# Kernel tuning notes

Hardware: AMD Instinct MI355X
Metric: run time of the kernel (lower is better)

The kernel has to match this reference:

```python
import jax, jax.numpy as jnp
import numpy as np

I_DIM = 50000
D_DIM = 128
N_EDGES = 800000
N_NODES = I_DIM + 1


def setup_inputs() -> dict:
    key = jax.random.key(0)
    k1, k2, k3, k4 = jax.random.split(key, 4)
    # edge[:,0] must be sorted for the original bincount+repeat normalization to be valid
    src = jnp.sort(jax.random.randint(k1, (N_EDGES,), 0, N_NODES))
    dst = jax.random.randint(k2, (N_EDGES,), 0, N_NODES)
    edge = jnp.stack([src, dst], axis=1).astype(jnp.int64)
    # GlorotNormal-style init for the embedding table and dense layers
    emb_mat = jax.random.normal(k3, (N_NODES, D_DIM), dtype=jnp.float32) * np.sqrt(2.0 / (N_NODES + D_DIM))
    kA, kB = jax.random.split(k4)
    W_scale = jax.random.normal(kA, (D_DIM, D_DIM), dtype=jnp.float32) * np.sqrt(2.0 / (2 * D_DIM))
    b_scale = jnp.zeros((D_DIM,), dtype=jnp.float32)
    W_att = jax.random.normal(kB, (2 * D_DIM, 1), dtype=jnp.float32) * np.sqrt(2.0 / (2 * D_DIM + 1))
    b_att = jnp.zeros((1,), dtype=jnp.float32)
    return {"edge": edge, "emb_mat": emb_mat, "W_scale": W_scale,
            "b_scale": b_scale, "W_att": W_att, "b_att": b_att}


def reference(edge, emb_mat, W_scale, b_scale, W_att, b_att):
    E = edge.shape[0]
    src = edge[:, 0]
    dst = edge[:, 1]
    # gather both endpoints, project: [E, 2, d]
    edge_emb = jnp.einsum('epd,df->epf', emb_mat[edge], W_scale) + b_scale
    edge_emb = edge_emb.reshape(E, -1)                       # [E, 2d]
    att = edge_emb @ W_att + b_att                           # [E, 1]
    att = jnp.where(att >= 0, att, 0.2 * att)                # LeakyReLU(0.2)
    att = jnp.squeeze(att, axis=-1)                          # [E]
    scores = jnp.exp(att - 1.0)
    score_sum = jax.ops.segment_sum(scores, src, num_segments=N_NODES)
    score_norm = scores / score_sum[src]                     # segment softmax
    item_scaled = emb_mat @ W_scale + b_scale                # [N, d]
    msgs = score_norm[:, None] * item_scaled[dst]            # [E, d]
    agg = jax.ops.segment_sum(msgs, src, num_segments=N_NODES)
    return jax.nn.sigmoid(agg)                               # [N, d]
```

## Files before the change

### kernel.cpp

```cpp
#include <hip/hip_runtime.h>
#include <math.h>

#define NN 50001
#define DD 128
#define NE 800000

typedef __attribute__((ext_vector_type(8))) short short8;
typedef __attribute__((ext_vector_type(4))) float floatx4;

__device__ __forceinline__ unsigned short f2bf(float f) {
    unsigned u = __builtin_bit_cast(unsigned, f);
    u += 0x7fffu + ((u >> 16) & 1u);
    return (unsigned short)(u >> 16);
}
__device__ __forceinline__ float bflo(unsigned u) {
    return __builtin_bit_cast(float, u << 16);
}
__device__ __forceinline__ float bfhi(unsigned u) {
    return __builtin_bit_cast(float, u & 0xffff0000u);
}

__global__ void k_prep(const float* __restrict__ W, unsigned short* __restrict__ WT,
                       const int* __restrict__ edge, int* __restrict__ row_ptr) {
    int b = blockIdx.x;
    if (b < 64) {
        int idx = b * 256 + threadIdx.x;
        int k = idx >> 7, j = idx & 127;
        WT[j * DD + k] = f2bf(W[idx]);
    } else {
        int e = (b - 64) * 256 + threadIdx.x;
        if (e >= NE) return;
        int s = edge[2 * e];
        if (e == 0) {
            for (int n = 0; n <= s; n++) row_ptr[n] = 0;
        } else {
            int p = edge[2 * (e - 1)];
            for (int n = p + 1; n <= s; n++) row_ptr[n] = e;
        }
        if (e == NE - 1) {
            for (int n = s + 1; n <= NN; n++) row_ptr[n] = NE;
        }
    }
}

__global__ void __launch_bounds__(256) k_gemm(const float* __restrict__ emb,
        const unsigned short* __restrict__ WT, const float* __restrict__ b_scale,
        const float* __restrict__ W_att, unsigned short* __restrict__ item,
        float* __restrict__ a_src, float* __restrict__ a_dst) {
    int wave = blockIdx.x * 4 + (threadIdx.x >> 6);
    int lane = threadIdx.x & 63;
    int base = wave * 16;
    if (base >= NN) return;
    int m = lane & 15, q = lane >> 4;

    int row = base + m; if (row >= NN) row = NN - 1;
    const float* ap = emb + (long)row * DD + q * 8;
    short8 a[4];
    #pragma unroll
    for (int ks = 0; ks < 4; ks++) {
        float4 f0 = *(const float4*)(ap + ks * 32);
        float4 f1 = *(const float4*)(ap + ks * 32 + 4);
        a[ks][0] = (short)f2bf(f0.x); a[ks][1] = (short)f2bf(f0.y);
        a[ks][2] = (short)f2bf(f0.z); a[ks][3] = (short)f2bf(f0.w);
        a[ks][4] = (short)f2bf(f1.x); a[ks][5] = (short)f2bf(f1.y);
        a[ks][6] = (short)f2bf(f1.z); a[ks][7] = (short)f2bf(f1.w);
    }

    float p_src[4] = {0.f, 0.f, 0.f, 0.f};
    float p_dst[4] = {0.f, 0.f, 0.f, 0.f};

    #pragma unroll
    for (int ft = 0; ft < 8; ft++) {
        int col = ft * 16 + m;
        floatx4 acc = {0.f, 0.f, 0.f, 0.f};
        #pragma unroll
        for (int ks = 0; ks < 4; ks++) {
            short8 b = *(const short8*)(WT + col * DD + ks * 32 + q * 8);
            acc = __builtin_amdgcn_mfma_f32_16x16x32_bf16(a[ks], b, acc, 0, 0, 0);
        }
        float bs = b_scale[col];
        float wsrc = W_att[col], wdst = W_att[DD + col];
        #pragma unroll
        for (int r = 0; r < 4; r++) {
            float v = acc[r] + bs;
            int gr = base + q * 4 + r;
            if (gr < NN) item[(long)gr * DD + col] = f2bf(v);
            p_src[r] += v * wsrc;
            p_dst[r] += v * wdst;
        }
    }
    #pragma unroll
    for (int off = 1; off <= 8; off <<= 1) {
        #pragma unroll
        for (int r = 0; r < 4; r++) {
            p_src[r] += __shfl_xor(p_src[r], off, 64);
            p_dst[r] += __shfl_xor(p_dst[r], off, 64);
        }
    }
    if (m == 0) {
        #pragma unroll
        for (int r = 0; r < 4; r++) {
            int gr = base + q * 4 + r;
            if (gr < NN) { a_src[gr] = p_src[r]; a_dst[gr] = p_dst[r]; }
        }
    }
}

__global__ void __launch_bounds__(256) k_score(const int* __restrict__ edge,
        const float* __restrict__ a_src, const float* __restrict__ a_dst,
        const float* __restrict__ b_att, uint2* __restrict__ sd) {
    int e = blockIdx.x * 256 + threadIdx.x;
    if (e >= NE) return;
    int2 ed = ((const int2*)edge)[e];
    float att = a_src[ed.x] + a_dst[ed.y] + b_att[0];
    att = att >= 0.f ? att : 0.2f * att;
    float s = __expf(att - 1.f);
    sd[e] = make_uint2((unsigned)ed.y, __builtin_bit_cast(unsigned, s));
}

__global__ void __launch_bounds__(256) k_agg(const int* __restrict__ row_ptr,
        const uint2* __restrict__ sd, const unsigned short* __restrict__ item,
        float* __restrict__ out) {
    int n = blockIdx.x * 4 + (threadIdx.x >> 6);
    int lane = threadIdx.x & 63;
    if (n >= NN) return;
    int g = lane >> 4, t = lane & 15;

    int start = row_ptr[n];
    int len = row_ptr[n + 1] - start;

    if (len > 0) {
        float acc[8] = {0.f, 0.f, 0.f, 0.f, 0.f, 0.f, 0.f, 0.f};
        float ssum = 0.f;
        const uint2* sp = sd + start;
        #pragma unroll 2
        for (int j = g; j < len; j += 4) {
            uint2 p = sp[j];
            float sj = __builtin_bit_cast(float, p.y);
            ssum += sj;
            const uint4 u = *(const uint4*)(item + (long)p.x * DD + t * 8);
            acc[0] += sj * bflo(u.x); acc[1] += sj * bfhi(u.x);
            acc[2] += sj * bflo(u.y); acc[3] += sj * bfhi(u.y);
            acc[4] += sj * bflo(u.z); acc[5] += sj * bfhi(u.z);
            acc[6] += sj * bflo(u.w); acc[7] += sj * bfhi(u.w);
        }
        #pragma unroll
        for (int off = 16; off <= 32; off <<= 1) {
            #pragma unroll
            for (int k = 0; k < 8; k++) acc[k] += __shfl_xor(acc[k], off, 64);
            ssum += __shfl_xor(ssum, off, 64);
        }
        float inv = 1.f / ssum;
        float4 o;
        if (g == 0) {
            o.x = 1.f / (1.f + __expf(-acc[0] * inv));
            o.y = 1.f / (1.f + __expf(-acc[1] * inv));
            o.z = 1.f / (1.f + __expf(-acc[2] * inv));
            o.w = 1.f / (1.f + __expf(-acc[3] * inv));
            *(float4*)(out + (long)n * DD + t * 8) = o;
        } else if (g == 1) {
            o.x = 1.f / (1.f + __expf(-acc[4] * inv));
            o.y = 1.f / (1.f + __expf(-acc[5] * inv));
            o.z = 1.f / (1.f + __expf(-acc[6] * inv));
            o.w = 1.f / (1.f + __expf(-acc[7] * inv));
            *(float4*)(out + (long)n * DD + t * 8 + 4) = o;
        }
    } else {
        float4 h = make_float4(0.5f, 0.5f, 0.5f, 0.5f);
        if (g == 0)      *(float4*)(out + (long)n * DD + t * 8) = h;
        else if (g == 1) *(float4*)(out + (long)n * DD + t * 8 + 4) = h;
    }
}

extern "C" void kernel_launch(void* const* d_in, const int* in_sizes, int n_in,
                              void* d_out, int out_size, void* d_ws, size_t ws_size,
                              hipStream_t stream) {
    const int*   edge    = (const int*)d_in[0];
    const float* emb     = (const float*)d_in[1];
    const float* W_scale = (const float*)d_in[2];
    const float* b_scale = (const float*)d_in[3];
    const float* W_att   = (const float*)d_in[4];
    const float* b_att   = (const float*)d_in[5];
    float* out = (float*)d_out;

    char* ws = (char*)d_ws;
    unsigned short* WT      = (unsigned short*)(ws);
    int*            row_ptr = (int*)(ws + 32768);
    float*          a_src   = (float*)(ws + 233600);
    float*          a_dst   = (float*)(ws + 433792);
    unsigned short* item    = (unsigned short*)(ws + 633984);
    uint2*          sd      = (uint2*)(ws + 13434240);

    int node_blocks = (NN + 3) / 4;
    int tile_blocks = ((NN + 15) / 16 + 3) / 4;
    int edge_blocks = (NE + 255) / 256;

    k_prep <<<64 + edge_blocks, 256, 0, stream>>>(W_scale, WT, edge, row_ptr);
    k_gemm <<<tile_blocks,      256, 0, stream>>>(emb, WT, b_scale, W_att, item, a_src, a_dst);
    k_score<<<edge_blocks,      256, 0, stream>>>(edge, a_src, a_dst, b_att, sd);
    k_agg  <<<node_blocks,      256, 0, stream>>>(row_ptr, sd, item, out);
}
```

Before: 146.3 us.

## Fuse edge score computation into aggregation kernel and unroll gather loop by four

Removes the separate per-edge score kernel and its intermediate (dst, score) buffer. The aggregation kernel now reads dst indices straight from the edge array, looks up a_dst, and computes the LeakyReLU/exp score inline. The main loop handles four edges per lane group per iteration so more independent gathers are in flight. This saves one launch and a write plus re-read of 6.4 MB of scratch. In exchange each of the 16 lanes in a group recomputes the exp redundantly and does an extra dependent a_dst gather.

```diff
diff --git a/kernel.cpp b/kernel.cpp
--- a/kernel.cpp
+++ b/kernel.cpp
@@ -18,6 +18,10 @@
 }
 __device__ __forceinline__ float bfhi(unsigned u) {
     return __builtin_bit_cast(float, u & 0xffff0000u);
+}
+__device__ __forceinline__ float score(float att) {
+    att = att >= 0.f ? att : 0.2f * att;
+    return __expf(att - 1.f);
 }
 
 __global__ void k_prep(const float* __restrict__ W, unsigned short* __restrict__ WT,
@@ -106,21 +110,10 @@
     }
 }
 
-__global__ void __launch_bounds__(256) k_score(const int* __restrict__ edge,
+__global__ void __launch_bounds__(256) k_agg(const int* __restrict__ edge,
+        const int* __restrict__ row_ptr, const unsigned short* __restrict__ item,
         const float* __restrict__ a_src, const float* __restrict__ a_dst,
-        const float* __restrict__ b_att, uint2* __restrict__ sd) {
-    int e = blockIdx.x * 256 + threadIdx.x;
-    if (e >= NE) return;
-    int2 ed = ((const int2*)edge)[e];
-    float att = a_src[ed.x] + a_dst[ed.y] + b_att[0];
-    att = att >= 0.f ? att : 0.2f * att;
-    float s = __expf(att - 1.f);
-    sd[e] = make_uint2((unsigned)ed.y, __builtin_bit_cast(unsigned, s));
-}
-
-__global__ void __launch_bounds__(256) k_agg(const int* __restrict__ row_ptr,
-        const uint2* __restrict__ sd, const unsigned short* __restrict__ item,
-        float* __restrict__ out) {
+        const float* __restrict__ b_att, float* __restrict__ out) {
     int n = blockIdx.x * 4 + (threadIdx.x >> 6);
     int lane = threadIdx.x & 63;
     if (n >= NN) return;
@@ -128,21 +121,50 @@
 
     int start = row_ptr[n];
     int len = row_ptr[n + 1] - start;
+    const int* dp = edge + 2 * start + 1;
 
     if (len > 0) {
+        float asrc = a_src[n] + b_att[0];
         float acc[8] = {0.f, 0.f, 0.f, 0.f, 0.f, 0.f, 0.f, 0.f};
         float ssum = 0.f;
-        const uint2* sp = sd + start;
-        #pragma unroll 2
-        for (int j = g; j < len; j += 4) {
-            uint2 p = sp[j];
-            float sj = __builtin_bit_cast(float, p.y);
-            ssum += sj;
-            const uint4 u = *(const uint4*)(item + (long)p.x * DD + t * 8);
-            acc[0] += sj * bflo(u.x); acc[1] += sj * bfhi(u.x);
-            acc[2] += sj * bflo(u.y); acc[3] += sj * bfhi(u.y);
-            acc[4] += sj * bflo(u.z); acc[5] += sj * bfhi(u.z);
-            acc[6] += sj * bflo(u.w); acc[7] += sj * bfhi(u.w);
+        int j = g;
+        for (; j + 12 < len; j += 16) {
+            int d0 = dp[2 * j], d1 = dp[2 * (j + 4)], d2 = dp[2 * (j + 8)], d3 = dp[2 * (j + 12)];
+            float x0 = a_dst[d0], x1 = a_dst[d1], x2 = a_dst[d2], x3 = a_dst[d3];
+            uint4 u0 = *(const uint4*)(item + (long)d0 * DD + t * 8);
+            uint4 u1 = *(const uint4*)(item + (long)d1 * DD + t * 8);
+            uint4 u2 = *(const uint4*)(item + (long)d2 * DD + t * 8);
+            uint4 u3 = *(const uint4*)(item + (long)d3 * DD + t * 8);
+            float s0 = score(asrc + x0), s1 = score(asrc + x1);
+            float s2 = score(asrc + x2), s3 = score(asrc + x3);
+            ssum += (s0 + s1) + (s2 + s3);
+            acc[0] += s0 * bflo(u0.x); acc[1] += s0 * bfhi(u0.x);
+            acc[2] += s0 * bflo(u0.y); acc[3] += s0 * bfhi(u0.y);
+            acc[4] += s0 * bflo(u0.z); acc[5] += s0 * bfhi(u0.z);
+            acc[6] += s0 * bflo(u0.w); acc[7] += s0 * bfhi(u0.w);
+            acc[0] += s1 * bflo(u1.x); acc[1] += s1 * bfhi(u1.x);
+            acc[2] += s1 * bflo(u1.y); acc[3] += s1 * bfhi(u1.y);
+            acc[4] += s1 * bflo(u1.z); acc[5] += s1 * bfhi(u1.z);
+            acc[6] += s1 * bflo(u1.w); acc[7] += s1 * bfhi(u1.w);
+            acc[0] += s2 * bflo(u2.x); acc[1] += s2 * bfhi(u2.x);
+            acc[2] += s2 * bflo(u2.y); acc[3] += s2 * bfhi(u2.y);
+            acc[4] += s2 * bflo(u2.z); acc[5] += s2 * bfhi(u2.z);
+            acc[6] += s2 * bflo(u2.w); acc[7] += s2 * bfhi(u2.w);
+            acc[0] += s3 * bflo(u3.x); acc[1] += s3 * bfhi(u3.x);
+            acc[2] += s3 * bflo(u3.y); acc[3] += s3 * bfhi(u3.y);
+            acc[4] += s3 * bflo(u3.z); acc[5] += s3 * bfhi(u3.z);
+            acc[6] += s3 * bflo(u3.w); acc[7] += s3 * bfhi(u3.w);
+        }
+        for (; j < len; j += 4) {
+            int d = dp[2 * j];
+            float x = a_dst[d];
+            uint4 u = *(const uint4*)(item + (long)d * DD + t * 8);
+            float s = score(asrc + x);
+            ssum += s;
+            acc[0] += s * bflo(u.x); acc[1] += s * bfhi(u.x);
+            acc[2] += s * bflo(u.y); acc[3] += s * bfhi(u.y);
+            acc[4] += s * bflo(u.z); acc[5] += s * bfhi(u.z);
+            acc[6] += s * bflo(u.w); acc[7] += s * bfhi(u.w);
         }
         #pragma unroll
         for (int off = 16; off <= 32; off <<= 1) {
@@ -189,7 +211,6 @@
     float*          a_src   = (float*)(ws + 233600);
     float*          a_dst   = (float*)(ws + 433792);
     unsigned short* item    = (unsigned short*)(ws + 633984);
-    uint2*          sd      = (uint2*)(ws + 13434240);
 
     int node_blocks = (NN + 3) / 4;
     int tile_blocks = ((NN + 15) / 16 + 3) / 4;
@@ -197,6 +218,5 @@
 
     k_prep <<<64 + edge_blocks, 256, 0, stream>>>(W_scale, WT, edge, row_ptr);
     k_gemm <<<tile_blocks,      256, 0, stream>>>(emb, WT, b_scale, W_att, item, a_src, a_dst);
-    k_score<<<edge_blocks,      256, 0, stream>>>(edge, a_src, a_dst, b_att, sd);
-    k_agg  <<<node_blocks,      256, 0, stream>>>(row_ptr, sd, item, out);
-}
+    k_agg  <<<node_blocks,      256, 0, stream>>>(edge, row_ptr, item, a_src, a_dst, b_att, out);
+}
```

Result: no change. 146.8 us (+0.3%).
